# Kernel optimization log

Measured on AMD Instinct MI355X. Metric: run time of the kernel, lower is better.

The kernel has to match this reference:

```python
import jax, jax.numpy as jnp
import numpy as np
from jax.scipy.special import logsumexp

B, N = 256, 65536
NEG_INF = jnp.float32(-1e30)  # acts as -inf for logsumexp, keeps grads finite


def setup_inputs() -> dict:
    key = jax.random.key(0)
    k1, k2 = jax.random.split(key)
    sim = jax.random.uniform(k1, (B, N), dtype=jnp.float32)
    label = jax.random.uniform(k2, (B, N), dtype=jnp.float32)
    return {"sim": sim, "label": label}


def _ranking_loss(sim, label):
    m = 0.2
    gamma = 64.0
    delta_p = 1.0 - m  # 0.8
    delta_n = m        # 0.2

    pos_mask = label > 0.5
    neg_mask = label < 0.25

    # ---- positives: logit_p = -relu(0.8 - sim).detach() * (sim - 0.8) * gamma ----
    alpha_p = jax.lax.stop_gradient(jnp.maximum(0.8 - sim, 0.0))
    logit_p = -alpha_p * (sim - delta_p) * gamma
    lse_p = logsumexp(jnp.where(pos_mask, logit_p, NEG_INF), axis=1)
    # torch fallback: no positives -> logit_p = [0.0], logsumexp == 0
    lse_p = jnp.where(pos_mask.any(axis=1), lse_p, 0.0)

    # ---- negatives: if >20 negatives, keep only top-10 largest sims ----
    alpha_n_all = jax.lax.stop_gradient(jnp.maximum(sim - 0.2, 0.0))
    logit_n_all = alpha_n_all * (sim - delta_n) * gamma
    lse_n_all = logsumexp(jnp.where(neg_mask, logit_n_all, NEG_INF), axis=1)

    neg_sim_masked = jnp.where(neg_mask, sim, NEG_INF)
    top_v, _ = jax.lax.top_k(neg_sim_masked, 10)  # [B, 10]
    alpha_n_top = jax.lax.stop_gradient(jnp.maximum(top_v - 0.2, 0.0))
    logit_n_top = alpha_n_top * (top_v - delta_n) * gamma
    lse_n_top = logsumexp(logit_n_top, axis=1)

    n_neg = neg_mask.sum(axis=1)
    lse_n = jnp.where(n_neg > 20, lse_n_top, lse_n_all)

    loss_loc = jax.nn.softplus(lse_n + lse_p).sum()
    return loss_loc / sim.shape[0]  # reduction='mean'


def reference(sim, label):
    return _ranking_loss(sim, label)
```

## Files before the change

kernel.cpp:

```cpp
#include <hip/hip_runtime.h>
#include <cmath>

#define NEG_INF (-1.0e30f)

static constexpr int B = 256;
static constexpr int N = 65536;
static constexpr int CHUNKS = 8;
static constexpr int THREADS = 256;
static constexpr int NBLOCKS = B * CHUNKS;
static constexpr int CHUNK_ELEMS = N / CHUNKS;
static constexpr int ITER = CHUNK_ELEMS / 4 / THREADS;
static constexpr float C_OFF = 40.96f;
static constexpr float CAND_THRESH = 0.98f;
static constexpr int CAP = 512;
static constexpr int PSTRIDE = 16;

__device__ __forceinline__ float wave_sum_f(float v) {
#pragma unroll
  for (int off = 32; off >= 1; off >>= 1) v += __shfl_xor(v, off, 64);
  return v;
}
__device__ __forceinline__ int wave_sum_i(int v) {
#pragma unroll
  for (int off = 32; off >= 1; off >>= 1) v += __shfl_xor(v, off, 64);
  return v;
}
__device__ __forceinline__ int wave_max_i(int v) {
#pragma unroll
  for (int off = 32; off >= 1; off >>= 1) v = max(v, __shfl_xor(v, off, 64));
  return v;
}

__device__ __forceinline__ void insert10(float t[16], float s) {
  if (s > t[9]) {
    t[9] = s;
#pragma unroll
    for (int i = 9; i > 0; --i) {
      float a = t[i - 1], b = t[i];
      t[i - 1] = fmaxf(a, b);
      t[i] = fminf(a, b);
    }
  }
}

__device__ __forceinline__ void merge_lists_shfl(float t[16], int off) {
  float b[16];
#pragma unroll
  for (int i = 0; i < 16; ++i) b[i] = __shfl_xor(t[i], off, 64);
  float c[16];
#pragma unroll
  for (int i = 0; i < 16; ++i) c[i] = fmaxf(t[i], b[15 - i]);
#pragma unroll
  for (int s = 8; s >= 1; s >>= 1) {
#pragma unroll
    for (int i = 0; i < 16; ++i) {
      if ((i & s) == 0) {
        float lo = c[i], hi = c[i + s];
        c[i] = fmaxf(lo, hi);
        c[i + s] = fminf(lo, hi);
      }
    }
  }
#pragma unroll
  for (int i = 0; i < 16; ++i) t[i] = c[i];
}

__device__ __forceinline__ void proc(float s, float l, float& s_p, float& s_n,
                                     int& nn, int& cc, float c4[4]) {
  const bool pos = l > 0.5f;
  const bool neg = l < 0.25f;
  float d = pos ? (0.8f - s) : (s - 0.2f);
  float r = fmaxf(d, 0.f);
  float e = __expf(fmaf(64.f * r, r, -C_OFF));
  s_p += pos ? e : 0.f;
  s_n += neg ? e : 0.f;
  nn += neg ? 1 : 0;
  const bool isc = neg && (s > CAND_THRESH);
  cc += isc ? 1 : 0;
  float v = isc ? s : NEG_INF;
  float t = fmaxf(c4[3], v);
  c4[3] = fminf(c4[2], t);
  t = fmaxf(c4[2], t);
  c4[2] = fminf(c4[1], t);
  t = fmaxf(c4[1], t);
  c4[1] = fminf(c4[0], t);
  c4[0] = fmaxf(c4[0], t);
}

__global__ void __launch_bounds__(THREADS, 4) ranking_partial_kernel(
    const float* __restrict__ sim, const float* __restrict__ label,
    float* __restrict__ partials) {
  const int blk = blockIdx.x;
  const int row = blk >> 3;
  const int chunk = blk & 7;
  const int tid = threadIdx.x;
  const int wave = tid >> 6, lane = tid & 63;

  __shared__ float cand[CAP];
  __shared__ int cnt;
  __shared__ float ls_p[4], ls_n[4];
  __shared__ int ls_c[4], ls_cc[4], ls_ccmax[4];
  __shared__ float ltop[4][16];
  if (tid == 0) cnt = 0;
  __syncthreads();

  const size_t base4 = (size_t)row * (N / 4) + (size_t)chunk * (CHUNK_ELEMS / 4);
  const float4* sim4 = reinterpret_cast<const float4*>(sim) + base4;
  const float4* lab4 = reinterpret_cast<const float4*>(label) + base4;

  float4 S[ITER], L[ITER];
#pragma unroll
  for (int it = 0; it < ITER; ++it) {
    S[it] = sim4[it * THREADS + tid];
    L[it] = lab4[it * THREADS + tid];
  }

  float s_p = 0.f, s_n = 0.f;
  int nn = 0, cc = 0;
  float c4[4] = {NEG_INF, NEG_INF, NEG_INF, NEG_INF};

#pragma unroll
  for (int it = 0; it < ITER; ++it) {
    proc(S[it].x, L[it].x, s_p, s_n, nn, cc, c4);
    proc(S[it].y, L[it].y, s_p, s_n, nn, cc, c4);
    proc(S[it].z, L[it].z, s_p, s_n, nn, cc, c4);
    proc(S[it].w, L[it].w, s_p, s_n, nn, cc, c4);
  }

  const int nst = min(cc, 4);
  for (int i = 0; i < nst; ++i) {
    int p = atomicAdd(&cnt, 1);
    if (p < CAP) cand[p] = c4[i];
  }

  float sw_p = wave_sum_f(s_p);
  float sw_n = wave_sum_f(s_n);
  int nw = wave_sum_i(nn);
  int ccw = wave_sum_i(cc);
  int ccmx = wave_max_i(cc);
  if (lane == 0) {
    ls_p[wave] = sw_p;
    ls_n[wave] = sw_n;
    ls_c[wave] = nw;
    ls_cc[wave] = ccw;
    ls_ccmax[wave] = ccmx;
  }
  __syncthreads();

  float sp_tot = ls_p[0] + ls_p[1] + ls_p[2] + ls_p[3];
  float sn_tot = ls_n[0] + ls_n[1] + ls_n[2] + ls_n[3];
  const int nn_tot = ls_c[0] + ls_c[1] + ls_c[2] + ls_c[3];
  const int cc_tot = ls_cc[0] + ls_cc[1] + ls_cc[2] + ls_cc[3];
  const int cc_max = max(max(ls_ccmax[0], ls_ccmax[1]), max(ls_ccmax[2], ls_ccmax[3]));

  const bool bad = (cc_max > 4) || (cc_tot > CAP) || (cc_tot < 10 && cc_tot < nn_tot);

  float t[16];
#pragma unroll
  for (int i = 0; i < 16; ++i) t[i] = NEG_INF;

  float* P = partials + (size_t)blk * PSTRIDE;

  if (!bad) {
    if (wave == 0) {
      const int c = cnt < CAP ? cnt : CAP;
      for (int i = lane; i < c; i += 64) insert10(t, cand[i]);
#pragma unroll
      for (int off = 1; off < 64; off <<= 1) merge_lists_shfl(t, off);
      if (lane == 0) {
        P[0] = sp_tot;
        P[1] = sn_tot;
        P[2] = (float)nn_tot;
        P[3] = 0.f;
#pragma unroll
        for (int i = 0; i < 10; ++i) P[4 + i] = t[i];
      }
    }
  } else {
#pragma unroll
    for (int it = 0; it < ITER; ++it) {
      if (L[it].x < 0.25f) insert10(t, S[it].x);
      if (L[it].y < 0.25f) insert10(t, S[it].y);
      if (L[it].z < 0.25f) insert10(t, S[it].z);
      if (L[it].w < 0.25f) insert10(t, S[it].w);
    }
#pragma unroll
    for (int off = 1; off < 64; off <<= 1) merge_lists_shfl(t, off);
    if (lane == 0) {
#pragma unroll
      for (int i = 0; i < 16; ++i) ltop[wave][i] = t[i];
    }
    __syncthreads();
    if (wave == 0) {
      float m[16];
      if (lane < 4) {
#pragma unroll
        for (int i = 0; i < 16; ++i) m[i] = ltop[lane][i];
      } else {
#pragma unroll
        for (int i = 0; i < 16; ++i) m[i] = NEG_INF;
      }
      merge_lists_shfl(m, 1);
      merge_lists_shfl(m, 2);
      if (lane == 0) {
        P[0] = sp_tot;
        P[1] = sn_tot;
        P[2] = (float)nn_tot;
        P[3] = 0.f;
#pragma unroll
        for (int i = 0; i < 10; ++i) P[4 + i] = m[i];
      }
    }
  }
}

__global__ void __launch_bounds__(256) final_kernel(
    const float* __restrict__ partials, float* __restrict__ out) {
  const int r = threadIdx.x;
  float sp = 0.f, sn = 0.f, nnf = 0.f;
  float t[16];
#pragma unroll
  for (int i = 0; i < 16; ++i) t[i] = NEG_INF;
#pragma unroll
  for (int c = 0; c < CHUNKS; ++c) {
    const float* P = partials + (size_t)(r * CHUNKS + c) * PSTRIDE;
    sp += P[0];
    sn += P[1];
    nnf += P[2];
#pragma unroll
    for (int i = 0; i < 10; ++i) insert10(t, P[4 + i]);
  }

  float lse_p = (sp > 0.f) ? (C_OFF + __logf(sp)) : 0.f;
  float lse_n_all = (sn > 0.f) ? (C_OFF + __logf(sn)) : NEG_INF;

  float mx = NEG_INF;
  float lg[10];
#pragma unroll
  for (int i = 0; i < 10; ++i) {
    float v = t[i];
    float a = fmaxf(v - 0.2f, 0.f);
    float lo = a * (v - 0.2f) * 64.f;
    lg[i] = lo;
    mx = fmaxf(mx, lo);
  }
  float ss = 0.f;
#pragma unroll
  for (int i = 0; i < 10; ++i) ss += __expf(lg[i] - mx);
  float lse_n_top = mx + __logf(ss);

  float lse_n = (nnf > 20.5f) ? lse_n_top : lse_n_all;
  float x = lse_n + lse_p;
  float loss = fmaxf(x, 0.f) + log1pf(__expf(-fabsf(x)));

  loss = wave_sum_f(loss);
  __shared__ float ws[4];
  if ((r & 63) == 0) ws[r >> 6] = loss;
  __syncthreads();
  if (r == 0) out[0] = (ws[0] + ws[1] + ws[2] + ws[3]) * (1.0f / 256.0f);
}

extern "C" void kernel_launch(void* const* d_in, const int* in_sizes, int n_in,
                              void* d_out, int out_size, void* d_ws, size_t ws_size,
                              hipStream_t stream) {
  const float* sim = (const float*)d_in[0];
  const float* label = (const float*)d_in[1];
  float* out = (float*)d_out;
  float* partials = (float*)d_ws;
  ranking_partial_kernel<<<dim3(NBLOCKS), dim3(THREADS), 0, stream>>>(sim, label, partials);
  final_kernel<<<dim3(1), dim3(256), 0, stream>>>(partials, out);
}
```

Before: 161.2 us.

## Split rows into 16 chunks and add per-row merge kernel with SoA partials

Measured after the change: 157.6 us. 2.2% less time.

```diff
diff --git a/kernel.cpp b/kernel.cpp
--- a/kernel.cpp
+++ b/kernel.cpp
@@ -5,15 +5,15 @@
 
 static constexpr int B = 256;
 static constexpr int N = 65536;
-static constexpr int CHUNKS = 8;
+static constexpr int CHUNKS = 16;
 static constexpr int THREADS = 256;
 static constexpr int NBLOCKS = B * CHUNKS;
 static constexpr int CHUNK_ELEMS = N / CHUNKS;
 static constexpr int ITER = CHUNK_ELEMS / 4 / THREADS;
 static constexpr float C_OFF = 40.96f;
-static constexpr float CAND_THRESH = 0.98f;
+static constexpr float CAND_THRESH = 0.90f;
 static constexpr int CAP = 512;
-static constexpr int PSTRIDE = 16;
+static constexpr int NPART = 13;
 
 __device__ __forceinline__ float wave_sum_f(float v) {
 #pragma unroll
@@ -87,12 +87,12 @@
   c4[0] = fmaxf(c4[0], t);
 }
 
-__global__ void __launch_bounds__(THREADS, 4) ranking_partial_kernel(
+__global__ void __launch_bounds__(THREADS, 8) ranking_partial_kernel(
     const float* __restrict__ sim, const float* __restrict__ label,
     float* __restrict__ partials) {
   const int blk = blockIdx.x;
-  const int row = blk >> 3;
-  const int chunk = blk & 7;
+  const int row = blk >> 4;
+  const int chunk = blk & 15;
   const int tid = threadIdx.x;
   const int wave = tid >> 6, lane = tid & 63;
 
@@ -159,8 +159,6 @@
 #pragma unroll
   for (int i = 0; i < 16; ++i) t[i] = NEG_INF;
 
-  float* P = partials + (size_t)blk * PSTRIDE;
-
   if (!bad) {
     if (wave == 0) {
       const int c = cnt < CAP ? cnt : CAP;
@@ -168,12 +166,11 @@
 #pragma unroll
       for (int off = 1; off < 64; off <<= 1) merge_lists_shfl(t, off);
       if (lane == 0) {
-        P[0] = sp_tot;
-        P[1] = sn_tot;
-        P[2] = (float)nn_tot;
-        P[3] = 0.f;
-#pragma unroll
-        for (int i = 0; i < 10; ++i) P[4 + i] = t[i];
+        partials[0 * NBLOCKS + blk] = sp_tot;
+        partials[1 * NBLOCKS + blk] = sn_tot;
+        partials[2 * NBLOCKS + blk] = (float)nn_tot;
+#pragma unroll
+        for (int i = 0; i < 10; ++i) partials[(3 + i) * NBLOCKS + blk] = t[i];
       }
     }
   } else {
@@ -203,61 +200,76 @@
       merge_lists_shfl(m, 1);
       merge_lists_shfl(m, 2);
       if (lane == 0) {
-        P[0] = sp_tot;
-        P[1] = sn_tot;
-        P[2] = (float)nn_tot;
-        P[3] = 0.f;
-#pragma unroll
-        for (int i = 0; i < 10; ++i) P[4 + i] = m[i];
-      }
-    }
+        partials[0 * NBLOCKS + blk] = sp_tot;
+        partials[1 * NBLOCKS + blk] = sn_tot;
+        partials[2 * NBLOCKS + blk] = (float)nn_tot;
+#pragma unroll
+        for (int i = 0; i < 10; ++i) partials[(3 + i) * NBLOCKS + blk] = m[i];
+      }
+    }
+  }
+}
+
+__global__ void __launch_bounds__(64) row_kernel(
+    const float* __restrict__ partials, float* __restrict__ row_loss) {
+  const int row = blockIdx.x;
+  const int lane = threadIdx.x;
+  const bool act = lane < CHUNKS;
+  const int blk = row * CHUNKS + (act ? lane : 0);
+
+  float sp = act ? partials[0 * NBLOCKS + blk] : 0.f;
+  float sn = act ? partials[1 * NBLOCKS + blk] : 0.f;
+  float nnf = act ? partials[2 * NBLOCKS + blk] : 0.f;
+  float t[16];
+#pragma unroll
+  for (int i = 0; i < 10; ++i)
+    t[i] = act ? partials[(3 + i) * NBLOCKS + blk] : NEG_INF;
+#pragma unroll
+  for (int i = 10; i < 16; ++i) t[i] = NEG_INF;
+
+  sp = wave_sum_f(sp);
+  sn = wave_sum_f(sn);
+  nnf = wave_sum_f(nnf);
+  merge_lists_shfl(t, 1);
+  merge_lists_shfl(t, 2);
+  merge_lists_shfl(t, 4);
+  merge_lists_shfl(t, 8);
+
+  if (lane == 0) {
+    float lse_p = (sp > 0.f) ? (C_OFF + __logf(sp)) : 0.f;
+    float lse_n_all = (sn > 0.f) ? (C_OFF + __logf(sn)) : NEG_INF;
+
+    float mx = NEG_INF;
+    float lg[10];
+#pragma unroll
+    for (int i = 0; i < 10; ++i) {
+      float v = t[i];
+      float a = fmaxf(v - 0.2f, 0.f);
+      float lo = a * (v - 0.2f) * 64.f;
+      lg[i] = lo;
+      mx = fmaxf(mx, lo);
+    }
+    float ss = 0.f;
+#pragma unroll
+    for (int i = 0; i < 10; ++i) ss += __expf(lg[i] - mx);
+    float lse_n_top = mx + __logf(ss);
+
+    float lse_n = (nnf > 20.5f) ? lse_n_top : lse_n_all;
+    float x = lse_n + lse_p;
+    float loss = fmaxf(x, 0.f) + log1pf(__expf(-fabsf(x)));
+    row_loss[row] = loss;
   }
 }
 
 __global__ void __launch_bounds__(256) final_kernel(
-    const float* __restrict__ partials, float* __restrict__ out) {
-  const int r = threadIdx.x;
-  float sp = 0.f, sn = 0.f, nnf = 0.f;
-  float t[16];
-#pragma unroll
-  for (int i = 0; i < 16; ++i) t[i] = NEG_INF;
-#pragma unroll
-  for (int c = 0; c < CHUNKS; ++c) {
-    const float* P = partials + (size_t)(r * CHUNKS + c) * PSTRIDE;
-    sp += P[0];
-    sn += P[1];
-    nnf += P[2];
-#pragma unroll
-    for (int i = 0; i < 10; ++i) insert10(t, P[4 + i]);
-  }
-
-  float lse_p = (sp > 0.f) ? (C_OFF + __logf(sp)) : 0.f;
-  float lse_n_all = (sn > 0.f) ? (C_OFF + __logf(sn)) : NEG_INF;
-
-  float mx = NEG_INF;
-  float lg[10];
-#pragma unroll
-  for (int i = 0; i < 10; ++i) {
-    float v = t[i];
-    float a = fmaxf(v - 0.2f, 0.f);
-    float lo = a * (v - 0.2f) * 64.f;
-    lg[i] = lo;
-    mx = fmaxf(mx, lo);
-  }
-  float ss = 0.f;
-#pragma unroll
-  for (int i = 0; i < 10; ++i) ss += __expf(lg[i] - mx);
-  float lse_n_top = mx + __logf(ss);
-
-  float lse_n = (nnf > 20.5f) ? lse_n_top : lse_n_all;
-  float x = lse_n + lse_p;
-  float loss = fmaxf(x, 0.f) + log1pf(__expf(-fabsf(x)));
-
-  loss = wave_sum_f(loss);
+    const float* __restrict__ row_loss, float* __restrict__ out) {
+  const int tid = threadIdx.x;
+  float v = row_loss[tid];
+  v = wave_sum_f(v);
   __shared__ float ws[4];
-  if ((r & 63) == 0) ws[r >> 6] = loss;
+  if ((tid & 63) == 0) ws[tid >> 6] = v;
   __syncthreads();
-  if (r == 0) out[0] = (ws[0] + ws[1] + ws[2] + ws[3]) * (1.0f / 256.0f);
+  if (tid == 0) out[0] = (ws[0] + ws[1] + ws[2] + ws[3]) * (1.0f / 256.0f);
 }
 
 extern "C" void kernel_launch(void* const* d_in, const int* in_sizes, int n_in,
@@ -267,6 +279,8 @@
   const float* label = (const float*)d_in[1];
   float* out = (float*)d_out;
   float* partials = (float*)d_ws;
+  float* rows = partials + NPART * NBLOCKS;
   ranking_partial_kernel<<<dim3(NBLOCKS), dim3(THREADS), 0, stream>>>(sim, label, partials);
-  final_kernel<<<dim3(1), dim3(256), 0, stream>>>(partials, out);
-}
+  row_kernel<<<dim3(B), dim3(64), 0, stream>>>(partials, rows);
+  final_kernel<<<dim3(1), dim3(256), 0, stream>>>(rows, out);
+}
```
